# Performance work log

Measured on AMD Instinct MI355X. Metric: run time of the kernel, lower is better.

## Reference

```python
import jax, jax.numpy as jnp
import numpy as np

ALPHA = 1.0


def _bce_with_logits(x, y):
    # torch BCEWithLogitsLoss (mean): y*softplus(-x) + (1-y)*softplus(x)
    return jnp.mean(y * jax.nn.softplus(-x) + (1.0 - y) * jax.nn.softplus(x))


def _cross_entropy(logits, labels):
    # torch CrossEntropyLoss (mean) with int class labels
    logp = jax.nn.log_softmax(logits, axis=-1)
    return -jnp.mean(jnp.take_along_axis(logp, labels[:, None], axis=-1))


def setup_inputs() -> dict:
    key = jax.random.key(0)
    ks = jax.random.split(key, 6)
    B, T, C = 2097152, 4, 16
    return {
        "y_pred_binary": jax.random.normal(ks[0], (B,), dtype=jnp.float32),
        "y_pred_type": jax.random.normal(ks[1], (B, T), dtype=jnp.float32),
        "y_pred_source": jax.random.normal(ks[2], (B, C), dtype=jnp.float32),
        "y_true_binary": jnp.round(jax.random.uniform(ks[3], (B,), dtype=jnp.float32)),
        "y_true_type": jnp.round(jax.random.uniform(ks[4], (B, T), dtype=jnp.float32)),
        "y_true_source": jax.random.randint(ks[5], (B,), 0, C, dtype=jnp.int32),
    }


def reference(y_pred_binary, y_pred_type, y_pred_source,
              y_true_binary, y_true_type, y_true_source):
    loss = _bce_with_logits(y_pred_binary, y_true_binary)
    loss = loss + _bce_with_logits(y_pred_type, y_true_type)
    loss = loss + _cross_entropy(y_pred_source, y_true_source)

    # Non-differentiable consistency counts (torch computes these under
    # no_grad / via round+argmax, which carry no gradient).
    pb = jax.lax.stop_gradient(y_pred_binary)
    pt = jax.lax.stop_gradient(y_pred_type)
    ps = jax.lax.stop_gradient(y_pred_source)

    binary_c = jax.nn.sigmoid(pb) >= 0.5                     # [B] bool (round(sigmoid))
    type_c = jnp.any(jax.nn.sigmoid(pt) >= 0.5, axis=1)      # [B] bool
    source_c = jnp.argmax(ps, axis=1) > 0                    # [B] bool

    # XOR: exactly one of the pair active -> inconsistent
    cons_ab = jnp.mean((binary_c ^ type_c).astype(jnp.float32))
    cons_ac = jnp.mean((binary_c ^ source_c).astype(jnp.float32))

    loss = loss + ALPHA * cons_ab + ALPHA * cons_ac
    return loss
```

## Files before the change

kernel.cpp:

```cpp
#include <hip/hip_runtime.h>
#include <math.h>

#define L2E 1.44269504088896340736f
#define LN2 0.69314718055994530942f

#if __has_builtin(__builtin_amdgcn_exp2f)
__device__ __forceinline__ float fexp2(float x)  { return __builtin_amdgcn_exp2f(x); }
#else
__device__ __forceinline__ float fexp2(float x)  { return __exp2f(x); }
#endif
#if __has_builtin(__builtin_amdgcn_logf)
__device__ __forceinline__ float flog2(float x)  { return __builtin_amdgcn_logf(x); }
#else
__device__ __forceinline__ float flog2(float x)  { return __log2f(x); }
#endif

__device__ __forceinline__ float row_contrib_full(
    const float* __restrict__ pb, const float4* __restrict__ pt4,
    const float4* __restrict__ ps4, const float* __restrict__ tb,
    const float4* __restrict__ tt4, const int* __restrict__ ts,
    const float* __restrict__ psf, int row)
{
    float  xb = pb[row], yb = tb[row];
    int    lab = ts[row];
    float4 xt = pt4[row], yt = tt4[row];
    size_t b = (size_t)row * 4;
    float4 r0 = ps4[b+0], r1 = ps4[b+1], r2 = ps4[b+2], r3 = ps4[b+3];
    float vlab = psf[(size_t)row * 16 + lab];
    float v[16] = { r0.x,r0.y,r0.z,r0.w, r1.x,r1.y,r1.z,r1.w,
                    r2.x,r2.y,r2.z,r2.w, r3.x,r3.y,r3.z,r3.w };
    float s = 0.0f;
    for (int j = 0; j < 16; ++j) s += fexp2(v[j] * L2E);
    float g = fexp2(xb * L2E);
    float p = (1.0f+fexp2(xt.x*L2E))*(1.0f+fexp2(xt.y*L2E))
            * (1.0f+fexp2(xt.z*L2E))*(1.0f+fexp2(xt.w*L2E));
    float c = LN2 * (flog2(s * (1.0f+g)) + 0.25f * flog2(p));
    float dot = xt.x*yt.x + xt.y*yt.y + xt.z*yt.z + xt.w*yt.w;
    c = c - vlab - yb*xb - 0.25f*dot;
    bool bin_c  = (xb >= 0.0f);
    bool type_c = fmaxf(fmaxf(xt.x,xt.y), fmaxf(xt.z,xt.w)) >= 0.0f;
    float mr = v[1];
    for (int j = 2; j < 16; ++j) mr = fmaxf(mr, v[j]);
    bool src_c = (mr > v[0]);
    c += (bin_c != type_c) ? 1.0f : 0.0f;
    c += (bin_c != src_c)  ? 1.0f : 0.0f;
    return c;
}

__global__ __launch_bounds__(256) void multitask_loss_kernel(
    const float*  __restrict__ pb,
    const float4* __restrict__ pt4,
    const float4* __restrict__ ps4,
    const float*  __restrict__ tb,
    const float4* __restrict__ tt4,
    const int*    __restrict__ ts,
    const float*  __restrict__ psf,
    float*        __restrict__ partials)
{
    const int tid = threadIdx.x;
    const int row = blockIdx.x * 256 + tid;

    float  xb = pb[row], yb = tb[row];
    int    lab = ts[row];
    float4 xt = pt4[row], yt = tt4[row];
    size_t b = (size_t)row * 4;
    float4 r0 = ps4[b+0], r1 = ps4[b+1], r2 = ps4[b+2], r3 = ps4[b+3];
    float  vlab = psf[(size_t)row * 16 + lab];

    float v[16] = { r0.x,r0.y,r0.z,r0.w, r1.x,r1.y,r1.z,r1.w,
                    r2.x,r2.y,r2.z,r2.w, r3.x,r3.y,r3.z,r3.w };

    float e[16];
    #pragma unroll
    for (int j = 0; j < 16; ++j) e[j] = fexp2(v[j] * L2E);
    #pragma unroll
    for (int st = 8; st >= 1; st >>= 1)
        #pragma unroll
        for (int j = 0; j < st; ++j) e[j] += e[j + st];
    float s = e[0];

    float g = fexp2(xb * L2E);
    float s2 = s * (1.0f + g);

    float f0 = fexp2(xt.x * L2E), f1 = fexp2(xt.y * L2E);
    float f2 = fexp2(xt.z * L2E), f3 = fexp2(xt.w * L2E);
    float p = ((1.0f+f0)*(1.0f+f1)) * ((1.0f+f2)*(1.0f+f3));

    float c = LN2 * (flog2(s2) + 0.25f * flog2(p));

    float dot = xt.x*yt.x + xt.y*yt.y + xt.z*yt.z + xt.w*yt.w;
    c = c - vlab - yb*xb - 0.25f*dot;

    bool bin_c  = (xb >= 0.0f);
    bool type_c = fmaxf(fmaxf(xt.x, xt.y), fmaxf(xt.z, xt.w)) >= 0.0f;
    float m01 = fmaxf(v[1],  v[2]),  m23 = fmaxf(v[3],  v[4]);
    float m45 = fmaxf(v[5],  v[6]),  m67 = fmaxf(v[7],  v[8]);
    float m89 = fmaxf(v[9],  v[10]), mab = fmaxf(v[11], v[12]);
    float mcd = fmaxf(v[13], v[14]);
    float mr  = fmaxf(fmaxf(fmaxf(m01, m23), fmaxf(m45, m67)),
                      fmaxf(fmaxf(m89, mab), fmaxf(mcd, v[15])));
    bool src_c = (mr > v[0]);

    unsigned long long mb = __ballot(bin_c);
    unsigned long long mt = __ballot(type_c);
    unsigned long long ms = __ballot(src_c);
    int pen = __popcll(mb ^ mt) + __popcll(mb ^ ms);

    #pragma unroll
    for (int off = 32; off > 0; off >>= 1)
        c += __shfl_down(c, off, 64);

    __shared__ float wsum[4];
    const int lane = tid & 63;
    const int wave = tid >> 6;
    if (lane == 0) wsum[wave] = c + (float)pen;
    __syncthreads();
    if (tid == 0)
        partials[blockIdx.x] = wsum[0] + wsum[1] + wsum[2] + wsum[3];
}

__global__ __launch_bounds__(256) void reduce_kernel(
    const float* __restrict__ partials, int nblocks,
    const float*  __restrict__ pb,  const float4* __restrict__ pt4,
    const float4* __restrict__ ps4, const float*  __restrict__ tb,
    const float4* __restrict__ tt4, const int*    __restrict__ ts,
    const float*  __restrict__ psf,
    int n_main, int B, float* __restrict__ out, double invB)
{
    double s = 0.0;
    for (int i = threadIdx.x; i < nblocks; i += 256)
        s += (double)partials[i];
    for (int r = n_main + threadIdx.x; r < B; r += 256)
        s += (double)row_contrib_full(pb, pt4, ps4, tb, tt4, ts, psf, r);

    #pragma unroll
    for (int off = 32; off > 0; off >>= 1)
        s += __shfl_down(s, off, 64);

    __shared__ double wsum[4];
    int lane = threadIdx.x & 63;
    int wave = threadIdx.x >> 6;
    if (lane == 0) wsum[wave] = s;
    __syncthreads();
    if (threadIdx.x == 0)
        out[0] = (float)((wsum[0] + wsum[1] + wsum[2] + wsum[3]) * invB);
}

extern "C" void kernel_launch(void* const* d_in, const int* in_sizes, int n_in,
                              void* d_out, int out_size, void* d_ws, size_t ws_size,
                              hipStream_t stream) {
    const float*  pb  = (const float*)d_in[0];
    const float4* pt4 = (const float4*)d_in[1];
    const float4* ps4 = (const float4*)d_in[2];
    const float*  psf = (const float*)d_in[2];
    const float*  tb  = (const float*)d_in[3];
    const float4* tt4 = (const float4*)d_in[4];
    const int*    ts  = (const int*)d_in[5];
    int B = in_sizes[0];

    float* partials = (float*)d_ws;

    int grid   = B / 256;
    int n_main = grid * 256;

    multitask_loss_kernel<<<grid, 256, 0, stream>>>(pb, pt4, ps4, tb, tt4, ts,
                                                    psf, partials);
    reduce_kernel<<<1, 256, 0, stream>>>(partials, grid,
                                         pb, pt4, ps4, tb, tt4, ts, psf,
                                         n_main, B, (float*)d_out,
                                         1.0 / (double)B);
}
```

Measured before the change: 262.6 us.

## Coalesce source-logit loads with quad-cooperative lane layout and grid-stride blocks

Result: no change. 259.4 us (-1.2%).

```diff
diff --git a/kernel.cpp b/kernel.cpp
--- a/kernel.cpp
+++ b/kernel.cpp
@@ -3,6 +3,7 @@
 
 #define L2E 1.44269504088896340736f
 #define LN2 0.69314718055994530942f
+#define G_BLOCKS 2048
 
 #if __has_builtin(__builtin_amdgcn_exp2f)
 __device__ __forceinline__ float fexp2(float x)  { return __builtin_amdgcn_exp2f(x); }
@@ -54,66 +55,87 @@
     const float*  __restrict__ tb,
     const float4* __restrict__ tt4,
     const int*    __restrict__ ts,
-    const float*  __restrict__ psf,
+    int iters,
     float*        __restrict__ partials)
 {
-    const int tid = threadIdx.x;
-    const int row = blockIdx.x * 256 + tid;
+    const int tid  = threadIdx.x;
+    const int lane = tid & 63;
+    const int wave = tid >> 6;
+    const int qz   = lane & 3;
+    const int grp  = lane >> 2;
 
-    float  xb = pb[row], yb = tb[row];
-    int    lab = ts[row];
-    float4 xt = pt4[row], yt = tt4[row];
-    size_t b = (size_t)row * 4;
-    float4 r0 = ps4[b+0], r1 = ps4[b+1], r2 = ps4[b+2], r3 = ps4[b+3];
-    float  vlab = psf[(size_t)row * 16 + lab];
+    float acc = 0.0f;
 
-    float v[16] = { r0.x,r0.y,r0.z,r0.w, r1.x,r1.y,r1.z,r1.w,
-                    r2.x,r2.y,r2.z,r2.w, r3.x,r3.y,r3.z,r3.w };
+    for (int it = 0; it < iters; ++it) {
+        const size_t R = ((size_t)it * G_BLOCKS + blockIdx.x) * 256
+                       + (size_t)wave * 64;
+        const int row = (int)R + lane;
 
-    float e[16];
-    #pragma unroll
-    for (int j = 0; j < 16; ++j) e[j] = fexp2(v[j] * L2E);
-    #pragma unroll
-    for (int st = 8; st >= 1; st >>= 1)
+        float  xb = pb[row];
+        float  yb = tb[row];
+        int    lab = ts[row];
+        float4 xt = pt4[row];
+        float4 yt = tt4[row];
+
+        size_t pbase = R * 4;
+        float4 q0 = ps4[pbase +   0 + lane];
+        float4 q1 = ps4[pbase +  64 + lane];
+        float4 q2 = ps4[pbase + 128 + lane];
+        float4 q3 = ps4[pbase + 192 + lane];
+
+        float g  = fexp2(xb * L2E);
+        float f0 = fexp2(xt.x*L2E), f1 = fexp2(xt.y*L2E);
+        float f2 = fexp2(xt.z*L2E), f3 = fexp2(xt.w*L2E);
+        float p  = ((1.0f+f0)*(1.0f+f1)) * ((1.0f+f2)*(1.0f+f3));
+        float dot = xt.x*yt.x + xt.y*yt.y + xt.z*yt.z + xt.w*yt.w;
+        float c = LN2 * (flog2(1.0f+g) + 0.25f*flog2(p)) - yb*xb - 0.25f*dot;
+        bool bin_c  = (xb >= 0.0f);
+        bool type_c = fmaxf(fmaxf(xt.x,xt.y), fmaxf(xt.z,xt.w)) >= 0.0f;
+
+        float S_own = 1.0f, V_own = 0.0f;
         #pragma unroll
-        for (int j = 0; j < st; ++j) e[j] += e[j + st];
-    float s = e[0];
+        for (int j = 0; j < 4; ++j) {
+            float4 qj = (j==0) ? q0 : (j==1) ? q1 : (j==2) ? q2 : q3;
 
-    float g = fexp2(xb * L2E);
-    float s2 = s * (1.0f + g);
+            float e = fexp2(qj.x*L2E) + fexp2(qj.y*L2E)
+                    + fexp2(qj.z*L2E) + fexp2(qj.w*L2E);
 
-    float f0 = fexp2(xt.x * L2E), f1 = fexp2(xt.y * L2E);
-    float f2 = fexp2(xt.z * L2E), f3 = fexp2(xt.w * L2E);
-    float p = ((1.0f+f0)*(1.0f+f1)) * ((1.0f+f2)*(1.0f+f3));
+            float m4 = fmaxf(fmaxf(qj.x,qj.y), fmaxf(qj.z,qj.w));
+            float m3 = fmaxf(fmaxf(qj.y,qj.z), qj.w);
+            float Mloc = (qz == 0) ? m3 : m4;
 
-    float c = LN2 * (flog2(s2) + 0.25f * flog2(p));
+            int labj = __shfl(lab, 16*j + grp, 64);
+            float sA  = (labj & 1) ? qj.y : qj.x;
+            float sB  = (labj & 1) ? qj.w : qj.z;
+            float sel = (labj & 2) ? sB : sA;
+            float vlab = __shfl(sel, (lane & ~3) + (labj >> 2), 64);
 
-    float dot = xt.x*yt.x + xt.y*yt.y + xt.z*yt.z + xt.w*yt.w;
-    c = c - vlab - yb*xb - 0.25f*dot;
+            float t = e + __shfl_xor(e, 1, 64);
+            float S = t + __shfl_xor(t, 2, 64);
+            float u = fmaxf(Mloc, __shfl_xor(Mloc, 1, 64));
+            float M = fmaxf(u, __shfl_xor(u, 2, 64));
+            float v0 = __shfl(qj.x, lane & ~3, 64);
 
-    bool bin_c  = (xb >= 0.0f);
-    bool type_c = fmaxf(fmaxf(xt.x, xt.y), fmaxf(xt.z, xt.w)) >= 0.0f;
-    float m01 = fmaxf(v[1],  v[2]),  m23 = fmaxf(v[3],  v[4]);
-    float m45 = fmaxf(v[5],  v[6]),  m67 = fmaxf(v[7],  v[8]);
-    float m89 = fmaxf(v[9],  v[10]), mab = fmaxf(v[11], v[12]);
-    float mcd = fmaxf(v[13], v[14]);
-    float mr  = fmaxf(fmaxf(fmaxf(m01, m23), fmaxf(m45, m67)),
-                      fmaxf(fmaxf(m89, mab), fmaxf(mcd, v[15])));
-    bool src_c = (mr > v[0]);
+            float Ssgn = (M > v0) ? -S : S;
 
-    unsigned long long mb = __ballot(bin_c);
-    unsigned long long mt = __ballot(type_c);
-    unsigned long long ms = __ballot(src_c);
-    int pen = __popcll(mb ^ mt) + __popcll(mb ^ ms);
+            float Sb = __shfl(Ssgn, (lane & 15) * 4, 64);
+            float Vb = __shfl(vlab, (lane & 15) * 4, 64);
+            if ((lane >> 4) == j) { S_own = Sb; V_own = Vb; }
+        }
+
+        bool src_c = (S_own < 0.0f);
+        c += LN2 * flog2(fabsf(S_own)) - V_own;
+        c += (bin_c != type_c) ? 1.0f : 0.0f;
+        c += (bin_c != src_c)  ? 1.0f : 0.0f;
+        acc += c;
+    }
 
     #pragma unroll
     for (int off = 32; off > 0; off >>= 1)
-        c += __shfl_down(c, off, 64);
+        acc += __shfl_down(acc, off, 64);
 
     __shared__ float wsum[4];
-    const int lane = tid & 63;
-    const int wave = tid >> 6;
-    if (lane == 0) wsum[wave] = c + (float)pen;
+    if (lane == 0) wsum[wave] = acc;
     __syncthreads();
     if (tid == 0)
         partials[blockIdx.x] = wsum[0] + wsum[1] + wsum[2] + wsum[3];
@@ -160,12 +182,12 @@
 
     float* partials = (float*)d_ws;
 
-    int grid   = B / 256;
-    int n_main = grid * 256;
+    int iters  = B / (G_BLOCKS * 256);
+    int n_main = iters * G_BLOCKS * 256;
 
-    multitask_loss_kernel<<<grid, 256, 0, stream>>>(pb, pt4, ps4, tb, tt4, ts,
-                                                    psf, partials);
-    reduce_kernel<<<1, 256, 0, stream>>>(partials, grid,
+    multitask_loss_kernel<<<G_BLOCKS, 256, 0, stream>>>(pb, pt4, ps4, tb, tt4,
+                                                        ts, iters, partials);
+    reduce_kernel<<<1, 256, 0, stream>>>(partials, G_BLOCKS,
                                          pb, pt4, ps4, tb, tt4, ts, psf,
                                          n_main, B, (float*)d_out,
                                          1.0 / (double)B);
```

## Stage source logits through LDS with double-buffered async global_load_lds over 4 row chunks

Applied to the files above, without the earlier changes.

Result: no change. 259.9 us (-1.0%).

```diff
diff --git a/kernel.cpp b/kernel.cpp
--- a/kernel.cpp
+++ b/kernel.cpp
@@ -3,6 +3,7 @@
 
 #define L2E 1.44269504088896340736f
 #define LN2 0.69314718055994530942f
+#define ITERS 4
 
 #if __has_builtin(__builtin_amdgcn_exp2f)
 __device__ __forceinline__ float fexp2(float x)  { return __builtin_amdgcn_exp2f(x); }
@@ -14,6 +15,8 @@
 #else
 __device__ __forceinline__ float flog2(float x)  { return __log2f(x); }
 #endif
+
+#define WAITCNT_VM4 0xF74
 
 __device__ __forceinline__ float row_contrib_full(
     const float* __restrict__ pb, const float4* __restrict__ pt4,
@@ -50,70 +53,102 @@
 __global__ __launch_bounds__(256) void multitask_loss_kernel(
     const float*  __restrict__ pb,
     const float4* __restrict__ pt4,
-    const float4* __restrict__ ps4,
+    const float*  __restrict__ ps,
     const float*  __restrict__ tb,
     const float4* __restrict__ tt4,
     const int*    __restrict__ ts,
-    const float*  __restrict__ psf,
     float*        __restrict__ partials)
 {
-    const int tid = threadIdx.x;
-    const int row = blockIdx.x * 256 + tid;
-
-    float  xb = pb[row], yb = tb[row];
-    int    lab = ts[row];
-    float4 xt = pt4[row], yt = tt4[row];
-    size_t b = (size_t)row * 4;
-    float4 r0 = ps4[b+0], r1 = ps4[b+1], r2 = ps4[b+2], r3 = ps4[b+3];
-    float  vlab = psf[(size_t)row * 16 + lab];
-
-    float v[16] = { r0.x,r0.y,r0.z,r0.w, r1.x,r1.y,r1.z,r1.w,
-                    r2.x,r2.y,r2.z,r2.w, r3.x,r3.y,r3.z,r3.w };
-
-    float e[16];
+    __shared__ float lps[4][2][1024];
+
+    const int tid  = threadIdx.x;
+    const int lane = tid & 63;
+    const int wave = tid >> 6;
+    const size_t wbase = (size_t)blockIdx.x * 1024 + (size_t)wave * (64 * ITERS);
+
+    {
+        const float* g = ps + wbase * 16;
+        #pragma unroll
+        for (int j = 0; j < 4; ++j)
+            __builtin_amdgcn_global_load_lds(
+                (const __attribute__((address_space(1))) void*)(g + j*256 + lane*4),
+                (__attribute__((address_space(3))) void*)(&lps[wave][0][j*256]),
+                16, 0, 0);
+    }
+
+    const int rot0 = (lane + ((lane >> 4) & 1)) & 15;
+    float acc = 0.0f;
+
     #pragma unroll
-    for (int j = 0; j < 16; ++j) e[j] = fexp2(v[j] * L2E);
-    #pragma unroll
-    for (int st = 8; st >= 1; st >>= 1)
+    for (int c = 0; c < ITERS; ++c) {
+        const int row = (int)(wbase + c * 64) + lane;
+
+        float  xb = pb[row];
+        float  yb = tb[row];
+        int    lab = ts[row];
+        float4 xt = pt4[row];
+        float4 yt = tt4[row];
+        __builtin_amdgcn_sched_barrier(0);
+
+        if (c + 1 < ITERS) {
+            const float* g = ps + (wbase + (size_t)(c + 1) * 64) * 16;
+            float* l = &lps[wave][(c + 1) & 1][0];
+            #pragma unroll
+            for (int j = 0; j < 4; ++j)
+                __builtin_amdgcn_global_load_lds(
+                    (const __attribute__((address_space(1))) void*)(g + j*256 + lane*4),
+                    (__attribute__((address_space(3))) void*)(l + j*256),
+                    16, 0, 0);
+        }
+        __builtin_amdgcn_sched_barrier(0);
+
+        __builtin_amdgcn_s_waitcnt(WAITCNT_VM4);
+        __builtin_amdgcn_sched_barrier(0);
+
+        const float* lv = &lps[wave][c & 1][lane * 16];
+
+        float s0 = 0.0f, s1 = 0.0f;
+        float m0 = -INFINITY, m1 = -INFINITY;
+        float v0 = 0.0f;
         #pragma unroll
-        for (int j = 0; j < st; ++j) e[j] += e[j + st];
-    float s = e[0];
-
-    float g = fexp2(xb * L2E);
-    float s2 = s * (1.0f + g);
-
-    float f0 = fexp2(xt.x * L2E), f1 = fexp2(xt.y * L2E);
-    float f2 = fexp2(xt.z * L2E), f3 = fexp2(xt.w * L2E);
-    float p = ((1.0f+f0)*(1.0f+f1)) * ((1.0f+f2)*(1.0f+f3));
-
-    float c = LN2 * (flog2(s2) + 0.25f * flog2(p));
-
-    float dot = xt.x*yt.x + xt.y*yt.y + xt.z*yt.z + xt.w*yt.w;
-    c = c - vlab - yb*xb - 0.25f*dot;
-
-    bool bin_c  = (xb >= 0.0f);
-    bool type_c = fmaxf(fmaxf(xt.x, xt.y), fmaxf(xt.z, xt.w)) >= 0.0f;
-    float m01 = fmaxf(v[1],  v[2]),  m23 = fmaxf(v[3],  v[4]);
-    float m45 = fmaxf(v[5],  v[6]),  m67 = fmaxf(v[7],  v[8]);
-    float m89 = fmaxf(v[9],  v[10]), mab = fmaxf(v[11], v[12]);
-    float mcd = fmaxf(v[13], v[14]);
-    float mr  = fmaxf(fmaxf(fmaxf(m01, m23), fmaxf(m45, m67)),
-                      fmaxf(fmaxf(m89, mab), fmaxf(mcd, v[15])));
-    bool src_c = (mr > v[0]);
-
-    unsigned long long mb = __ballot(bin_c);
-    unsigned long long mt = __ballot(type_c);
-    unsigned long long ms = __ballot(src_c);
-    int pen = __popcll(mb ^ mt) + __popcll(mb ^ ms);
+        for (int d = 0; d < 16; ++d) {
+            int   cls = (d + rot0) & 15;
+            float val = lv[cls];
+            if (d & 1) { s1 += fexp2(val * L2E); m1 = fmaxf(m1, val); }
+            else       { s0 += fexp2(val * L2E); m0 = fmaxf(m0, val); }
+            v0 = (cls == 0) ? val : v0;
+        }
+        float S    = s0 + s1;
+        float mall = fmaxf(m0, m1);
+        float vlab = lv[lab];
+
+        float g  = fexp2(xb * L2E);
+        float f0 = fexp2(xt.x*L2E), f1 = fexp2(xt.y*L2E);
+        float f2 = fexp2(xt.z*L2E), f3 = fexp2(xt.w*L2E);
+        float p  = ((1.0f+f0)*(1.0f+f1)) * ((1.0f+f2)*(1.0f+f3));
+
+        float dot = xt.x*yt.x + xt.y*yt.y + xt.z*yt.z + xt.w*yt.w;
+        float cc = LN2 * (flog2(S * (1.0f + g)) + 0.25f * flog2(p))
+                 - vlab - yb*xb - 0.25f*dot;
+
+        bool bin_c  = (xb >= 0.0f);
+        bool type_c = fmaxf(fmaxf(xt.x, xt.y), fmaxf(xt.z, xt.w)) >= 0.0f;
+        bool src_c  = (mall > v0);
+
+        unsigned long long mb = __ballot(bin_c);
+        unsigned long long mt = __ballot(type_c);
+        unsigned long long ms = __ballot(src_c);
+        int pen = __popcll(mb ^ mt) + __popcll(mb ^ ms);
+
+        acc += cc + (float)pen * (1.0f / 64.0f);
+    }
 
     #pragma unroll
     for (int off = 32; off > 0; off >>= 1)
-        c += __shfl_down(c, off, 64);
+        acc += __shfl_down(acc, off, 64);
 
     __shared__ float wsum[4];
-    const int lane = tid & 63;
-    const int wave = tid >> 6;
-    if (lane == 0) wsum[wave] = c + (float)pen;
+    if (lane == 0) wsum[wave] = acc;
     __syncthreads();
     if (tid == 0)
         partials[blockIdx.x] = wsum[0] + wsum[1] + wsum[2] + wsum[3];
@@ -151,8 +186,8 @@
                               hipStream_t stream) {
     const float*  pb  = (const float*)d_in[0];
     const float4* pt4 = (const float4*)d_in[1];
+    const float*  psf = (const float*)d_in[2];
     const float4* ps4 = (const float4*)d_in[2];
-    const float*  psf = (const float*)d_in[2];
     const float*  tb  = (const float*)d_in[3];
     const float4* tt4 = (const float4*)d_in[4];
     const int*    ts  = (const int*)d_in[5];
@@ -160,12 +195,12 @@
 
     float* partials = (float*)d_ws;
 
-    int grid   = B / 256;
-    int n_main = grid * 256;
-
-    multitask_loss_kernel<<<grid, 256, 0, stream>>>(pb, pt4, ps4, tb, tt4, ts,
-                                                    psf, partials);
-    reduce_kernel<<<1, 256, 0, stream>>>(partials, grid,
+    int blocks = B / 1024;
+    int n_main = blocks * 1024;
+
+    multitask_loss_kernel<<<blocks, 256, 0, stream>>>(pb, pt4, psf, tb, tt4, ts,
+                                                      partials);
+    reduce_kernel<<<1, 256, 0, stream>>>(partials, blocks,
                                          pb, pt4, ps4, tb, tt4, ts, psf,
                                          n_main, B, (float*)d_out,
                                          1.0 / (double)B);
```

## Split fused loss kernel into per-task kernels with ballot masks

Applied to the files above, without the earlier changes.

Result: no change. 262.8 us (+0.1%).

```diff
diff --git a/kernel.cpp b/kernel.cpp
--- a/kernel.cpp
+++ b/kernel.cpp
@@ -3,6 +3,9 @@
 
 #define L2E 1.44269504088896340736f
 #define LN2 0.69314718055994530942f
+#define NBLK 2048
+#define NTHR 256
+#define NWAVES (NBLK * (NTHR / 64))
 
 #if __has_builtin(__builtin_amdgcn_exp2f)
 __device__ __forceinline__ float fexp2(float x)  { return __builtin_amdgcn_exp2f(x); }
@@ -14,6 +17,20 @@
 #else
 __device__ __forceinline__ float flog2(float x)  { return __log2f(x); }
 #endif
+
+__device__ __forceinline__ void block_reduce_store(float v, float* __restrict__ partials)
+{
+    #pragma unroll
+    for (int off = 32; off > 0; off >>= 1)
+        v += __shfl_down(v, off, 64);
+    __shared__ float wsum[4];
+    const int lane = threadIdx.x & 63;
+    const int wave = threadIdx.x >> 6;
+    if (lane == 0) wsum[wave] = v;
+    __syncthreads();
+    if (threadIdx.x == 0)
+        partials[blockIdx.x] = wsum[0] + wsum[1] + wsum[2] + wsum[3];
+}
 
 __device__ __forceinline__ float row_contrib_full(
     const float* __restrict__ pb, const float4* __restrict__ pt4,
@@ -47,80 +64,95 @@
     return c;
 }
 
-__global__ __launch_bounds__(256) void multitask_loss_kernel(
-    const float*  __restrict__ pb,
-    const float4* __restrict__ pt4,
-    const float4* __restrict__ ps4,
-    const float*  __restrict__ tb,
-    const float4* __restrict__ tt4,
-    const int*    __restrict__ ts,
-    const float*  __restrict__ psf,
-    float*        __restrict__ partials)
-{
-    const int tid = threadIdx.x;
-    const int row = blockIdx.x * 256 + tid;
-
-    float  xb = pb[row], yb = tb[row];
-    int    lab = ts[row];
-    float4 xt = pt4[row], yt = tt4[row];
-    size_t b = (size_t)row * 4;
-    float4 r0 = ps4[b+0], r1 = ps4[b+1], r2 = ps4[b+2], r3 = ps4[b+3];
-    float  vlab = psf[(size_t)row * 16 + lab];
-
-    float v[16] = { r0.x,r0.y,r0.z,r0.w, r1.x,r1.y,r1.z,r1.w,
-                    r2.x,r2.y,r2.z,r2.w, r3.x,r3.y,r3.z,r3.w };
-
-    float e[16];
-    #pragma unroll
-    for (int j = 0; j < 16; ++j) e[j] = fexp2(v[j] * L2E);
-    #pragma unroll
-    for (int st = 8; st >= 1; st >>= 1)
+__global__ __launch_bounds__(256) void type_kernel(
+    const float4* __restrict__ pt4, const float4* __restrict__ tt4,
+    unsigned long long* __restrict__ tmask, float* __restrict__ part, int ngrp)
+{
+    const int lane = threadIdx.x & 63;
+    const int wid0 = blockIdx.x * (NTHR / 64) + (threadIdx.x >> 6);
+    float acc = 0.0f;
+    for (int g = wid0; g < ngrp; g += NWAVES) {
+        int row = g * 64 + lane;
+        float4 xt = pt4[row];
+        float4 yt = tt4[row];
+        float f0 = fexp2(xt.x*L2E), f1 = fexp2(xt.y*L2E);
+        float f2 = fexp2(xt.z*L2E), f3 = fexp2(xt.w*L2E);
+        float p  = ((1.0f+f0)*(1.0f+f1)) * ((1.0f+f2)*(1.0f+f3));
+        float dot = xt.x*yt.x + xt.y*yt.y + xt.z*yt.z + xt.w*yt.w;
+        acc += 0.25f * (LN2 * flog2(p) - dot);
+        bool type_c = fmaxf(fmaxf(xt.x, xt.y), fmaxf(xt.z, xt.w)) >= 0.0f;
+        unsigned long long m = __ballot(type_c);
+        if (lane == 0) tmask[g] = m;
+    }
+    block_reduce_store(acc, part);
+}
+
+__global__ __launch_bounds__(256) void src_kernel(
+    const float4* __restrict__ ps4, const float* __restrict__ psf,
+    const int* __restrict__ ts,
+    unsigned long long* __restrict__ smask, float* __restrict__ part, int ngrp)
+{
+    const int lane = threadIdx.x & 63;
+    const int wid0 = blockIdx.x * (NTHR / 64) + (threadIdx.x >> 6);
+    float acc = 0.0f;
+    for (int g = wid0; g < ngrp; g += NWAVES) {
+        int row = g * 64 + lane;
+        int lab = ts[row];
+        size_t b = (size_t)row * 4;
+        float4 r0 = ps4[b+0], r1 = ps4[b+1], r2 = ps4[b+2], r3 = ps4[b+3];
+        float vlab = psf[(size_t)row * 16 + lab];
+
+        float v[16] = { r0.x,r0.y,r0.z,r0.w, r1.x,r1.y,r1.z,r1.w,
+                        r2.x,r2.y,r2.z,r2.w, r3.x,r3.y,r3.z,r3.w };
+        float e[16];
         #pragma unroll
-        for (int j = 0; j < st; ++j) e[j] += e[j + st];
-    float s = e[0];
-
-    float g = fexp2(xb * L2E);
-    float s2 = s * (1.0f + g);
-
-    float f0 = fexp2(xt.x * L2E), f1 = fexp2(xt.y * L2E);
-    float f2 = fexp2(xt.z * L2E), f3 = fexp2(xt.w * L2E);
-    float p = ((1.0f+f0)*(1.0f+f1)) * ((1.0f+f2)*(1.0f+f3));
-
-    float c = LN2 * (flog2(s2) + 0.25f * flog2(p));
-
-    float dot = xt.x*yt.x + xt.y*yt.y + xt.z*yt.z + xt.w*yt.w;
-    c = c - vlab - yb*xb - 0.25f*dot;
-
-    bool bin_c  = (xb >= 0.0f);
-    bool type_c = fmaxf(fmaxf(xt.x, xt.y), fmaxf(xt.z, xt.w)) >= 0.0f;
-    float m01 = fmaxf(v[1],  v[2]),  m23 = fmaxf(v[3],  v[4]);
-    float m45 = fmaxf(v[5],  v[6]),  m67 = fmaxf(v[7],  v[8]);
-    float m89 = fmaxf(v[9],  v[10]), mab = fmaxf(v[11], v[12]);
-    float mcd = fmaxf(v[13], v[14]);
-    float mr  = fmaxf(fmaxf(fmaxf(m01, m23), fmaxf(m45, m67)),
-                      fmaxf(fmaxf(m89, mab), fmaxf(mcd, v[15])));
-    bool src_c = (mr > v[0]);
-
-    unsigned long long mb = __ballot(bin_c);
-    unsigned long long mt = __ballot(type_c);
-    unsigned long long ms = __ballot(src_c);
-    int pen = __popcll(mb ^ mt) + __popcll(mb ^ ms);
-
-    #pragma unroll
-    for (int off = 32; off > 0; off >>= 1)
-        c += __shfl_down(c, off, 64);
-
-    __shared__ float wsum[4];
-    const int lane = tid & 63;
-    const int wave = tid >> 6;
-    if (lane == 0) wsum[wave] = c + (float)pen;
-    __syncthreads();
-    if (tid == 0)
-        partials[blockIdx.x] = wsum[0] + wsum[1] + wsum[2] + wsum[3];
-}
-
-__global__ __launch_bounds__(256) void reduce_kernel(
-    const float* __restrict__ partials, int nblocks,
+        for (int j = 0; j < 16; ++j) e[j] = fexp2(v[j] * L2E);
+        #pragma unroll
+        for (int st = 8; st >= 1; st >>= 1)
+            #pragma unroll
+            for (int j = 0; j < st; ++j) e[j] += e[j + st];
+
+        acc += LN2 * flog2(e[0]) - vlab;
+
+        float m01 = fmaxf(v[1],  v[2]),  m23 = fmaxf(v[3],  v[4]);
+        float m45 = fmaxf(v[5],  v[6]),  m67 = fmaxf(v[7],  v[8]);
+        float m89 = fmaxf(v[9],  v[10]), mab = fmaxf(v[11], v[12]);
+        float mcd = fmaxf(v[13], v[14]);
+        float mr  = fmaxf(fmaxf(fmaxf(m01, m23), fmaxf(m45, m67)),
+                          fmaxf(fmaxf(m89, mab), fmaxf(mcd, v[15])));
+        bool src_c = (mr > v[0]);
+        unsigned long long m = __ballot(src_c);
+        if (lane == 0) smask[g] = m;
+    }
+    block_reduce_store(acc, part);
+}
+
+__global__ __launch_bounds__(256) void bin_kernel(
+    const float* __restrict__ pb, const float* __restrict__ tb,
+    const unsigned long long* __restrict__ tmask,
+    const unsigned long long* __restrict__ smask,
+    float* __restrict__ part, int ngrp)
+{
+    const int lane = threadIdx.x & 63;
+    const int wid0 = blockIdx.x * (NTHR / 64) + (threadIdx.x >> 6);
+    float acc = 0.0f;
+    for (int g = wid0; g < ngrp; g += NWAVES) {
+        int row = g * 64 + lane;
+        float xb = pb[row], yb = tb[row];
+        float gg = fexp2(xb * L2E);
+        acc += LN2 * flog2(1.0f + gg) - yb * xb;
+        unsigned long long mb = __ballot(xb >= 0.0f);
+        if (lane == 0) {
+            int pen = __popcll(mb ^ tmask[g]) + __popcll(mb ^ smask[g]);
+            acc += (float)pen;
+        }
+    }
+    block_reduce_store(acc, part);
+}
+
+__global__ __launch_bounds__(256) void final_kernel(
+    const float* __restrict__ part1, const float* __restrict__ part2,
+    const float* __restrict__ part3,
     const float*  __restrict__ pb,  const float4* __restrict__ pt4,
     const float4* __restrict__ ps4, const float*  __restrict__ tb,
     const float4* __restrict__ tt4, const int*    __restrict__ ts,
@@ -128,15 +160,14 @@
     int n_main, int B, float* __restrict__ out, double invB)
 {
     double s = 0.0;
-    for (int i = threadIdx.x; i < nblocks; i += 256)
-        s += (double)partials[i];
+    for (int i = threadIdx.x; i < NBLK; i += 256)
+        s += (double)part1[i] + (double)part2[i] + (double)part3[i];
     for (int r = n_main + threadIdx.x; r < B; r += 256)
         s += (double)row_contrib_full(pb, pt4, ps4, tb, tt4, ts, psf, r);
 
     #pragma unroll
     for (int off = 32; off > 0; off >>= 1)
         s += __shfl_down(s, off, 64);
-
     __shared__ double wsum[4];
     int lane = threadIdx.x & 63;
     int wave = threadIdx.x >> 6;
@@ -158,15 +189,21 @@
     const int*    ts  = (const int*)d_in[5];
     int B = in_sizes[0];
 
-    float* partials = (float*)d_ws;
-
-    int grid   = B / 256;
-    int n_main = grid * 256;
-
-    multitask_loss_kernel<<<grid, 256, 0, stream>>>(pb, pt4, ps4, tb, tt4, ts,
-                                                    psf, partials);
-    reduce_kernel<<<1, 256, 0, stream>>>(partials, grid,
-                                         pb, pt4, ps4, tb, tt4, ts, psf,
-                                         n_main, B, (float*)d_out,
-                                         1.0 / (double)B);
-}
+    float* part1 = (float*)d_ws;
+    float* part2 = part1 + NBLK;
+    float* part3 = part2 + NBLK;
+    unsigned long long* tmask =
+        (unsigned long long*)((char*)d_ws + 32 * 1024);
+    unsigned long long* smask = tmask + (B / 64);
+
+    int ngrp   = B / 64;
+    int n_main = ngrp * 64;
+
+    type_kernel<<<NBLK, NTHR, 0, stream>>>(pt4, tt4, tmask, part1, ngrp);
+    src_kernel <<<NBLK, NTHR, 0, stream>>>(ps4, psf, ts, smask, part2, ngrp);
+    bin_kernel <<<NBLK, NTHR, 0, stream>>>(pb, tb, tmask, smask, part3, ngrp);
+    final_kernel<<<1, 256, 0, stream>>>(part1, part2, part3,
+                                        pb, pt4, ps4, tb, tt4, ts, psf,
+                                        n_main, B, (float*)d_out,
+                                        1.0 / (double)B);
+}
```
